# Performance work log

Hardware: AMD Instinct MI355X
Metric: run time of the kernel (lower is better)

Reference implementation:

```python
import jax, jax.numpy as jnp
import numpy as np

N_NODES = 50000
N_EDGES = 800000
HID = 128
EDGE_IN = 2 * HID + 4 + 20  # 2*hidden + edge_feat_dim + num_r_gaussian = 280


def setup_inputs() -> dict:
    key = jax.random.key(0)
    ks = jax.random.split(key, 16)
    s = lambda fan_in: 1.0 / np.sqrt(fan_in)
    inp = {
        "h": jax.random.normal(ks[0], (N_NODES, HID), dtype=jnp.float32),
        "edge_index": jax.random.randint(ks[1], (2, N_EDGES), 0, N_NODES, dtype=jnp.int64) if jax.config.jax_enable_x64 else jax.random.randint(ks[1], (2, N_EDGES), 0, N_NODES, dtype=jnp.int32),
        "edge_attr": jax.random.normal(ks[2], (N_EDGES, 24), dtype=jnp.float32),
        # edge_mlp: Linear(280->128) relu Linear(128->128) relu (act_last=True)
        "We1": jax.random.uniform(ks[3], (EDGE_IN, HID), jnp.float32, -s(EDGE_IN), s(EDGE_IN)),
        "be1": jnp.zeros((HID,), jnp.float32),
        "We2": jax.random.uniform(ks[4], (HID, HID), jnp.float32, -s(HID), s(HID)),
        "be2": jnp.zeros((HID,), jnp.float32),
        # edge_inf: Linear(128->1) + sigmoid
        "Wg": jax.random.uniform(ks[5], (HID, 1), jnp.float32, -s(HID), s(HID)),
        "bg": jnp.zeros((1,), jnp.float32),
        # node_mlp: Linear(256->128) relu Linear(128->128)
        "Wn1": jax.random.uniform(ks[6], (2 * HID, HID), jnp.float32, -s(2 * HID), s(2 * HID)),
        "bn1": jnp.zeros((HID,), jnp.float32),
        "Wn2": jax.random.uniform(ks[7], (HID, HID), jnp.float32, -s(HID), s(HID)),
        "bn2": jnp.zeros((HID,), jnp.float32),
    }
    return inp


def reference(h, edge_index, edge_attr, We1, be1, We2, be2, Wg, bg, Wn1, bn1, Wn2, bn2):
    dst, src = edge_index[0], edge_index[1]
    hi, hj = h[dst], h[src]                       # [E, HID] each
    x = jnp.concatenate([edge_attr, hi, hj], -1)  # [E, 280]
    mij = jax.nn.relu(jax.nn.relu(x @ We1 + be1) @ We2 + be2)  # [E, HID]
    eij = jax.nn.sigmoid(mij @ Wg + bg)           # [E, 1]
    mi = jax.ops.segment_sum(mij * eij, dst, num_segments=h.shape[0])  # [N, HID]
    y = jnp.concatenate([mi, h], -1)              # [N, 2*HID]
    out = jax.nn.relu(y @ Wn1 + bn1) @ Wn2 + bn2  # [N, HID]
    return out
```

## Files before the change

kernel.cpp:

```cpp
#include <hip/hip_runtime.h>

#define N_NODES 50000
#define N_EDGES 800000
#define HID 128

typedef _Float16 f16;
typedef _Float16 half8 __attribute__((ext_vector_type(8)));
typedef _Float16 half4 __attribute__((ext_vector_type(4)));
typedef _Float16 half2v __attribute__((ext_vector_type(2)));
typedef float f32x4 __attribute__((ext_vector_type(4)));
typedef float f32x2 __attribute__((ext_vector_type(2)));

#define OFF_MI     0UL
#define OFF_H16C   25600000UL
#define OFF_WC     38400000UL
#define OFF_CNT    38604800UL
#define OFF_CUR    38805504UL
#define OFF_E4     39006208UL
#define OFF_BT     51806208UL
#define CSR_TOTAL  51806464UL

#define OFF_FMI  0UL
#define OFF_FH16 25600000UL
#define OFF_FW   38400000UL

#define WB1 0
#define WB2 36864
#define WN1 53248
#define WN2 86016

#define TS 136
#define YS 264
#define AS 40

#define EB 64
#define NB 32

__global__ __launch_bounds__(256) void pack_weights(
    const float* __restrict__ We1, const float* __restrict__ We2,
    const float* __restrict__ Wn1, const float* __restrict__ Wn2,
    f16* __restrict__ W, int* __restrict__ cnt, float* __restrict__ mi) {
  int i = blockIdx.x * 256 + threadIdx.x;
  if (cnt && i < 50176) cnt[i] = 0;
  if (mi) {
    f32x4 z = {0.f, 0.f, 0.f, 0.f};
    for (int j = i; j < N_NODES * HID / 4; j += 102400)
      ((f32x4*)mi)[j] = z;
  }
  if (i < 36864) {
    int j = i & 7, n = (i >> 3) & 127, qk = i >> 10;
    int k = qk * 8 + j;
    float v = 0.f;
    if (k < 256) v = We1[(24 + k) * 128 + n];
    else if (k < 280) v = We1[(k - 256) * 128 + n];
    W[WB1 + i] = (f16)v;
  } else if (i < 53248) {
    int l = i - 36864;
    int j = l & 7, n = (l >> 3) & 127, qk = l >> 10;
    W[WB2 + l] = (f16)We2[(qk * 8 + j) * 128 + n];
  } else if (i < 86016) {
    int l = i - 53248;
    int j = l & 7, n = (l >> 3) & 127, qk = l >> 10;
    W[WN1 + l] = (f16)Wn1[(qk * 8 + j) * 128 + n];
  } else if (i < 102400) {
    int l = i - 86016;
    int j = l & 7, n = (l >> 3) & 127, qk = l >> 10;
    W[WN2 + l] = (f16)Wn2[(qk * 8 + j) * 128 + n];
  }
}

__global__ __launch_bounds__(256) void scanA(const int* __restrict__ cnt,
                                             int* __restrict__ cur, int* __restrict__ bt) {
  __shared__ int wsum[4];
  int t = threadIdx.x, b = blockIdx.x;
  int base = b * 1024 + t * 4;
  int4 v = *(const int4*)(cnt + base);
  int s = v.x + v.y + v.z + v.w;
  int lane = t & 63, w = t >> 6;
  int inc = s;
  #pragma unroll
  for (int off = 1; off < 64; off <<= 1) {
    int u = __shfl_up(inc, off, 64);
    if (lane >= off) inc += u;
  }
  if (lane == 63) wsum[w] = inc;
  __syncthreads();
  int wbase = 0;
  for (int i = 0; i < w; ++i) wbase += wsum[i];
  int excl = wbase + inc - s;
  int4 o;
  o.x = excl; o.y = excl + v.x; o.z = o.y + v.y; o.w = o.z + v.z;
  *(int4*)(cur + base) = o;
  if (t == 255) bt[b] = wbase + inc;
}

__global__ __launch_bounds__(256) void scanC(int* __restrict__ cur, const int* __restrict__ bt) {
  __shared__ int sbase;
  int t = threadIdx.x, b = blockIdx.x;
  if (t < 64) {
    int v = (t < b) ? bt[t] : 0;
    #pragma unroll
    for (int off = 32; off; off >>= 1) v += __shfl_down(v, off, 64);
    if (t == 0) sbase = v;
  }
  __syncthreads();
  int add = sbase;
  int base = b * 1024 + t * 4;
  int4 o = *(int4*)(cur + base);
  o.x += add; o.y += add; o.z += add; o.w += add;
  *(int4*)(cur + base) = o;
}

__global__ __launch_bounds__(256) void fill_perm(
    const int* __restrict__ eidx, int* __restrict__ cur, int4* __restrict__ e4) {
  int i = blockIdx.x * 256 + threadIdx.x;
  int d = eidx[i];
  int s = eidx[N_EDGES + i];
  int p = atomicAdd(&cur[d], 1);
  int4 rec; rec.x = i; rec.y = d; rec.z = s; rec.w = 0;
  e4[p] = rec;
}

__global__ __launch_bounds__(256, 8) void precompute_kernel(
    const float* __restrict__ h, const int* __restrict__ eidx,
    const f16* __restrict__ Wp, f16* __restrict__ P,
    f16* __restrict__ h16, int* __restrict__ cnt) {
  __shared__ f16 Y[NB * 136];
  int t = threadIdx.x;
  int n0 = blockIdx.x * NB;
  {
    int rb = t >> 4, ch = t & 15;
    #pragma unroll
    for (int p = 0; p < 2; ++p) {
      int r = p * 16 + rb;
      int g = n0 + r; if (g >= N_NODES) g = N_NODES - 1;
      const float4* s4 = (const float4*)(h + (size_t)g * HID + ch * 8);
      float4 a = s4[0], b = s4[1];
      half8 v = {(f16)a.x, (f16)a.y, (f16)a.z, (f16)a.w,
                 (f16)b.x, (f16)b.y, (f16)b.z, (f16)b.w};
      *(half8*)&Y[r * 136 + ch * 8] = v;
      *(half8*)(h16 + (size_t)g * HID + ch * 8) = v;
    }
  }
  if (cnt) {
    for (int i = blockIdx.x * 256 + t; i < N_EDGES; i += gridDim.x * 256)
      atomicAdd(&cnt[eidx[i]], 1);
  }
  __syncthreads();
  int w = t >> 6, lane = t & 63, q = lane >> 4, c = lane & 15;
  int colBase = w * 32;
  const f16* B = Wp + WB1 + ((size_t)(q * 128 + colBase + c)) * 8;
  f32x4 aD[2][2], aS[2][2];
  #pragma unroll
  for (int mt = 0; mt < 2; ++mt) {
    aD[mt][0] = (f32x4){0, 0, 0, 0}; aD[mt][1] = (f32x4){0, 0, 0, 0};
    aS[mt][0] = (f32x4){0, 0, 0, 0}; aS[mt][1] = (f32x4){0, 0, 0, 0};
  }
  #pragma unroll
  for (int ks = 0; ks < 4; ++ks) {
    half8 bD0 = *(const half8*)(B + ks * 4096);
    half8 bD1 = *(const half8*)(B + ks * 4096 + 128);
    half8 bS0 = *(const half8*)(B + (ks + 4) * 4096);
    half8 bS1 = *(const half8*)(B + (ks + 4) * 4096 + 128);
    #pragma unroll
    for (int mt = 0; mt < 2; ++mt) {
      half8 a = *(const half8*)&Y[(mt * 16 + c) * 136 + ks * 32 + q * 8];
      aD[mt][0] = __builtin_amdgcn_mfma_f32_16x16x32_f16(a, bD0, aD[mt][0], 0, 0, 0);
      aD[mt][1] = __builtin_amdgcn_mfma_f32_16x16x32_f16(a, bD1, aD[mt][1], 0, 0, 0);
      aS[mt][0] = __builtin_amdgcn_mfma_f32_16x16x32_f16(a, bS0, aS[mt][0], 0, 0, 0);
      aS[mt][1] = __builtin_amdgcn_mfma_f32_16x16x32_f16(a, bS1, aS[mt][1], 0, 0, 0);
    }
  }
  #pragma unroll
  for (int mt = 0; mt < 2; ++mt)
    #pragma unroll
    for (int r = 0; r < 4; ++r) {
      int g = n0 + mt * 16 + q * 4 + r;
      if (g < N_NODES) {
        f16* o = P + (size_t)g * 256 + colBase + c;
        o[0]        = (f16)aD[mt][0][r];
        o[16]       = (f16)aD[mt][1][r];
        o[128]      = (f16)aS[mt][0][r];
        o[128 + 16] = (f16)aS[mt][1][r];
      }
    }
}

__global__ __launch_bounds__(256, 6) void edge_kernel(
    const f16* __restrict__ P, const int* __restrict__ eidx,
    const float* __restrict__ eattr,
    const f16* __restrict__ Wp, const float* __restrict__ be1,
    const float* __restrict__ be2,
    const float* __restrict__ Wg, const float* __restrict__ bg,
    float* __restrict__ mi, const int4* __restrict__ e4) {
  __shared__ f16 S16[EB * TS];
  __shared__ f16 A[EB * AS];
  __shared__ float part[EB * 4];
  __shared__ float eijL[EB];
  __shared__ int dstL[EB];
  int t = threadIdx.x;
  int e0 = blockIdx.x * EB;

  if (t < EB) dstL[t] = e4 ? e4[e0 + t].y : eidx[e0 + t];

  {
    int rb = t >> 4, ch = t & 15;
    #pragma unroll
    for (int p = 0; p < 4; ++p) {
      int r = p * 16 + rb;
      int d, s;
      if (e4) {
        int4 rec = e4[e0 + r];
        d = rec.y; s = rec.z;
      } else {
        d = eidx[e0 + r]; s = eidx[N_EDGES + e0 + r];
      }
      half8 pd = *(const half8*)(P + (size_t)d * 256 + ch * 8);
      half8 ps = *(const half8*)(P + (size_t)s * 256 + 128 + ch * 8);
      *(half8*)&S16[r * TS + ch * 8] = pd + ps;
    }
  }
  for (int i = t; i < 384; i += 256) {
    int el = i / 6, kk = i % 6;
    int e = e4 ? e4[e0 + el].x : (e0 + el);
    float4 f = *(const float4*)(eattr + (size_t)e * 24 + kk * 4);
    half4 hv = {(f16)f.x, (f16)f.y, (f16)f.z, (f16)f.w};
    *(half4*)&A[el * AS + kk * 4] = hv;
  }
  if (t < EB) { uint4 z = {0, 0, 0, 0}; *(uint4*)&A[t * AS + 24] = z; }
  __syncthreads();

  int w = t >> 6, lane = t & 63, q = lane >> 4, c = lane & 15;
  int colBase = w * 32;

  f32x4 acc[4][2];
  {
    float b0 = be1[colBase + c], b1 = be1[colBase + 16 + c];
    #pragma unroll
    for (int mt = 0; mt < 4; ++mt) {
      acc[mt][0] = (f32x4){b0, b0, b0, b0};
      acc[mt][1] = (f32x4){b1, b1, b1, b1};
    }
  }
  {
    const f16* bA = Wp + WB1 + 32768 + ((size_t)(q * 128 + colBase + c)) * 8;
    half8 b0f = *(const half8*)(bA);
    half8 b1f = *(const half8*)(bA + 128);
    #pragma unroll
    for (int mt = 0; mt < 4; ++mt) {
      half8 a = *(const half8*)&A[(mt * 16 + c) * AS + q * 8];
      acc[mt][0] = __builtin_amdgcn_mfma_f32_16x16x32_f16(a, b0f, acc[mt][0], 0, 0, 0);
      acc[mt][1] = __builtin_amdgcn_mfma_f32_16x16x32_f16(a, b1f, acc[mt][1], 0, 0, 0);
    }
  }
  #pragma unroll
  for (int mt = 0; mt < 4; ++mt)
    #pragma unroll
    for (int r = 0; r < 4; ++r) {
      const f16* sr = &S16[(mt * 16 + q * 4 + r) * TS + colBase + c];
      acc[mt][0][r] += (float)sr[0];
      acc[mt][1][r] += (float)sr[16];
    }

  const f16* bp2base = Wp + WB2 + ((size_t)(q * 128 + colBase + c)) * 8;
  half8 d0 = *(const half8*)(bp2base);
  half8 d1 = *(const half8*)(bp2base + 128);

  __syncthreads();
  f16* T = S16;
  #pragma unroll
  for (int mt = 0; mt < 4; ++mt)
    #pragma unroll
    for (int nt = 0; nt < 2; ++nt)
      #pragma unroll
      for (int r = 0; r < 4; ++r) {
        float v = acc[mt][nt][r];
        T[(mt * 16 + q * 4 + r) * TS + colBase + nt * 16 + c] = (f16)(v > 0.f ? v : 0.f);
      }
  __syncthreads();

  f32x4 m2[4][2];
  {
    float b0 = be2[colBase + c], b1 = be2[colBase + 16 + c];
    #pragma unroll
    for (int mt = 0; mt < 4; ++mt) {
      m2[mt][0] = (f32x4){b0, b0, b0, b0};
      m2[mt][1] = (f32x4){b1, b1, b1, b1};
    }
  }
  #pragma unroll
  for (int kk = 0; kk < 4; ++kk) {
    half8 n0, n1;
    if (kk < 3) {
      n0 = *(const half8*)(bp2base + (kk + 1) * 4096);
      n1 = *(const half8*)(bp2base + (kk + 1) * 4096 + 128);
    }
    #pragma unroll
    for (int mt = 0; mt < 4; ++mt) {
      half8 a = *(const half8*)&T[(mt * 16 + c) * TS + kk * 32 + q * 8];
      m2[mt][0] = __builtin_amdgcn_mfma_f32_16x16x32_f16(a, d0, m2[mt][0], 0, 0, 0);
      m2[mt][1] = __builtin_amdgcn_mfma_f32_16x16x32_f16(a, d1, m2[mt][1], 0, 0, 0);
    }
    d0 = n0; d1 = n1;
  }

  float wg0 = Wg[colBase + c], wg1 = Wg[colBase + 16 + c];
  float pd[4][4];
  #pragma unroll
  for (int mt = 0; mt < 4; ++mt)
    #pragma unroll
    for (int r = 0; r < 4; ++r) {
      float v0 = m2[mt][0][r]; v0 = v0 > 0.f ? v0 : 0.f; m2[mt][0][r] = v0;
      float v1 = m2[mt][1][r]; v1 = v1 > 0.f ? v1 : 0.f; m2[mt][1][r] = v1;
      pd[mt][r] = v0 * wg0 + v1 * wg1;
    }
  #pragma unroll
  for (int off = 1; off < 16; off <<= 1)
    #pragma unroll
    for (int mt = 0; mt < 4; ++mt)
      #pragma unroll
      for (int r = 0; r < 4; ++r)
        pd[mt][r] += __shfl_xor(pd[mt][r], off, 64);
  if (c == 0)
    #pragma unroll
    for (int mt = 0; mt < 4; ++mt)
      #pragma unroll
      for (int r = 0; r < 4; ++r)
        part[(mt * 16 + q * 4 + r) * 4 + w] = pd[mt][r];
  __syncthreads();
  if (t < EB) {
    float s = part[t * 4] + part[t * 4 + 1] + part[t * 4 + 2] + part[t * 4 + 3] + bg[0];
    eijL[t] = 1.f / (1.f + __expf(-s));
  }
  __syncthreads();

  if (e4) {
    #pragma unroll
    for (int mt = 0; mt < 4; ++mt)
      #pragma unroll
      for (int r = 0; r < 4; ++r) {
        int el = mt * 16 + q * 4 + r;
        float ev = eijL[el];
        T[el * TS + colBase + c]      = (f16)(m2[mt][0][r] * ev);
        T[el * TS + colBase + 16 + c] = (f16)(m2[mt][1][r] * ev);
      }
    __syncthreads();
    int col = t & 127, half = t >> 7;
    int r0 = half * 32;
    float acc2 = 0.f;
    int dprev = dstL[r0];
    #pragma unroll
    for (int r2 = 0; r2 < 32; ++r2) {
      int rr = r0 + r2;
      acc2 += (float)T[rr * TS + col];
      int dnext = (r2 == 31) ? -1 : dstL[rr + 1];
      if (dnext != dprev) {
        atomicAdd(&mi[(size_t)dprev * HID + col], acc2);
        acc2 = 0.f;
        dprev = dnext;
      }
    }
  } else {
    #pragma unroll
    for (int mt = 0; mt < 4; ++mt)
      #pragma unroll
      for (int r = 0; r < 4; ++r) {
        int el = mt * 16 + q * 4 + r;
        float ev = eijL[el];
        float* base = mi + (size_t)dstL[el] * HID + colBase + c;
        atomicAdd(base,      m2[mt][0][r] * ev);
        atomicAdd(base + 16, m2[mt][1][r] * ev);
      }
  }
}

__global__ __launch_bounds__(256, 8) void node_kernel(
    const float* __restrict__ mi, const f16* __restrict__ h16,
    const f16* __restrict__ Wp, const float* __restrict__ bn1,
    const float* __restrict__ bn2, float* __restrict__ out) {
  __shared__ f16 Y[NB * YS];
  int t = threadIdx.x;
  int n0 = blockIdx.x * NB;
  {
    int rb = t >> 4, ch = t & 15;
    #pragma unroll
    for (int p = 0; p < 2; ++p) {
      int r = p * 16 + rb;
      int g = n0 + r; if (g >= N_NODES) g = N_NODES - 1;
      const float4* s = (const float4*)(mi + (size_t)g * HID + ch * 8);
      float4 a = s[0], b = s[1];
      half8 v = {(f16)a.x, (f16)a.y, (f16)a.z, (f16)a.w,
                 (f16)b.x, (f16)b.y, (f16)b.z, (f16)b.w};
      *(half8*)&Y[r * YS + ch * 8] = v;
      *(uint4*)&Y[r * YS + 128 + ch * 8] = *(const uint4*)(h16 + (size_t)g * HID + ch * 8);
    }
  }
  __syncthreads();
  int w = t >> 6, lane = t & 63, q = lane >> 4, c = lane & 15;
  int colBase = w * 32;
  const f16* BN1 = Wp + WN1;
  const f16* BN2 = Wp + WN2;
  f32x4 acc[2][2];
  {
    float b0 = bn1[colBase + c], b1 = bn1[colBase + 16 + c];
    #pragma unroll
    for (int mt = 0; mt < 2; ++mt) {
      acc[mt][0] = (f32x4){b0, b0, b0, b0};
      acc[mt][1] = (f32x4){b1, b1, b1, b1};
    }
  }
  const f16* bn1base = BN1 + ((size_t)(q * 128 + colBase + c)) * 8;
  half8 bf0 = *(const half8*)(bn1base);
  half8 bf1 = *(const half8*)(bn1base + 128);
  #pragma unroll
  for (int ks = 0; ks < 8; ++ks) {
    half8 nb0, nb1;
    if (ks < 7) {
      nb0 = *(const half8*)(bn1base + (ks + 1) * 4096);
      nb1 = *(const half8*)(bn1base + (ks + 1) * 4096 + 128);
    }
    #pragma unroll
    for (int mt = 0; mt < 2; ++mt) {
      half8 a = *(const half8*)&Y[(mt * 16 + c) * YS + ks * 32 + q * 8];
      acc[mt][0] = __builtin_amdgcn_mfma_f32_16x16x32_f16(a, bf0, acc[mt][0], 0, 0, 0);
      acc[mt][1] = __builtin_amdgcn_mfma_f32_16x16x32_f16(a, bf1, acc[mt][1], 0, 0, 0);
    }
    bf0 = nb0; bf1 = nb1;
  }
  const f16* bn2base = BN2 + ((size_t)(q * 128 + colBase + c)) * 8;
  half8 d0 = *(const half8*)(bn2base);
  half8 d1 = *(const half8*)(bn2base + 128);
  __syncthreads();
  f16* T = Y;
  #pragma unroll
  for (int mt = 0; mt < 2; ++mt)
    #pragma unroll
    for (int nt = 0; nt < 2; ++nt)
      #pragma unroll
      for (int r = 0; r < 4; ++r) {
        float v = acc[mt][nt][r];
        T[(mt * 16 + q * 4 + r) * TS + colBase + nt * 16 + c] = (f16)(v > 0.f ? v : 0.f);
      }
  __syncthreads();
  f32x4 m2[2][2];
  {
    float b0 = bn2[colBase + c], b1 = bn2[colBase + 16 + c];
    #pragma unroll
    for (int mt = 0; mt < 2; ++mt) {
      m2[mt][0] = (f32x4){b0, b0, b0, b0};
      m2[mt][1] = (f32x4){b1, b1, b1, b1};
    }
  }
  #pragma unroll
  for (int kk = 0; kk < 4; ++kk) {
    half8 n0, n1;
    if (kk < 3) {
      n0 = *(const half8*)(bn2base + (kk + 1) * 4096);
      n1 = *(const half8*)(bn2base + (kk + 1) * 4096 + 128);
    }
    #pragma unroll
    for (int mt = 0; mt < 2; ++mt) {
      half8 a = *(const half8*)&T[(mt * 16 + c) * TS + kk * 32 + q * 8];
      m2[mt][0] = __builtin_amdgcn_mfma_f32_16x16x32_f16(a, d0, m2[mt][0], 0, 0, 0);
      m2[mt][1] = __builtin_amdgcn_mfma_f32_16x16x32_f16(a, d1, m2[mt][1], 0, 0, 0);
    }
    d0 = n0; d1 = n1;
  }
  #pragma unroll
  for (int mt = 0; mt < 2; ++mt)
    #pragma unroll
    for (int r = 0; r < 4; ++r) {
      int g = n0 + mt * 16 + q * 4 + r;
      if (g < N_NODES) {
        float* o = out + (size_t)g * HID + colBase + c;
        o[0]  = m2[mt][0][r];
        o[16] = m2[mt][1][r];
      }
    }
}

extern "C" void kernel_launch(void* const* d_in, const int* in_sizes, int n_in,
                              void* d_out, int out_size, void* d_ws, size_t ws_size,
                              hipStream_t stream) {
  const float* h    = (const float*)d_in[0];
  const int*   eidx = (const int*)d_in[1];
  const float* eattr= (const float*)d_in[2];
  const float* We1  = (const float*)d_in[3];
  const float* be1  = (const float*)d_in[4];
  const float* We2  = (const float*)d_in[5];
  const float* be2  = (const float*)d_in[6];
  const float* Wg   = (const float*)d_in[7];
  const float* bg   = (const float*)d_in[8];
  const float* Wn1  = (const float*)d_in[9];
  const float* bn1  = (const float*)d_in[10];
  const float* Wn2  = (const float*)d_in[11];
  const float* bn2  = (const float*)d_in[12];
  float* out = (float*)d_out;
  char* ws = (char*)d_ws;

  if (ws_size >= CSR_TOTAL) {
    float* mi  = (float*)(ws + OFF_MI);
    f16* h16   = (f16*)(ws + OFF_H16C);
    f16* Wp    = (f16*)(ws + OFF_WC);
    int* cnt   = (int*)(ws + OFF_CNT);
    int* cur   = (int*)(ws + OFF_CUR);
    int4* e4   = (int4*)(ws + OFF_E4);
    int* bt    = (int*)(ws + OFF_BT);
    f16* P     = (f16*)out;

    pack_weights<<<400, 256, 0, stream>>>(We1, We2, Wn1, Wn2, Wp, cnt, mi);
    precompute_kernel<<<(N_NODES + NB - 1) / NB, 256, 0, stream>>>(h, eidx, Wp, P, h16, cnt);
    scanA<<<49, 256, 0, stream>>>(cnt, cur, bt);
    scanC<<<49, 256, 0, stream>>>(cur, bt);
    fill_perm<<<3125, 256, 0, stream>>>(eidx, cur, e4);
    edge_kernel<<<N_EDGES / EB, 256, 0, stream>>>(P, eidx, eattr, Wp, be1, be2,
                                                  Wg, bg, mi, e4);
    node_kernel<<<(N_NODES + NB - 1) / NB, 256, 0, stream>>>(mi, h16, Wp, bn1, bn2, out);
  } else {
    float* mi  = (float*)(ws + OFF_FMI);
    f16*   h16 = (f16*)(ws + OFF_FH16);
    f16*   Wp  = (f16*)(ws + OFF_FW);
    f16*   P   = (f16*)out;

    pack_weights<<<400, 256, 0, stream>>>(We1, We2, Wn1, Wn2, Wp, nullptr, mi);
    precompute_kernel<<<(N_NODES + NB - 1) / NB, 256, 0, stream>>>(h, eidx, Wp, P, h16, nullptr);
    edge_kernel<<<N_EDGES / EB, 256, 0, stream>>>(P, eidx, eattr, Wp, be1, be2,
                                                  Wg, bg, mi, nullptr);
    node_kernel<<<(N_NODES + NB - 1) / NB, 256, 0, stream>>>(mi, h16, Wp, bn1, bn2, out);
  }
}
```

Before: 400.3 us.

## Halve edge tile, swizzle block order, merge scan kernels into one pass

Edge tiles shrink from 64 to 32 edges per block, and launch bounds rise to allow 8 waves-groups per CU. The block index is remapped so consecutive blocks take strided regions of the sorted edge list. The two-kernel prefix scan becomes a single kernel in which each block recomputes the sum of the preceding counts itself, removing one launch. The segmented atomic reduction now uses half2 reads over 8-row groups. Smaller tiles can mean more atomics per destination and less weight reuse per block.

```diff
diff --git a/kernel.cpp b/kernel.cpp
--- a/kernel.cpp
+++ b/kernel.cpp
@@ -17,8 +17,7 @@
 #define OFF_CNT    38604800UL
 #define OFF_CUR    38805504UL
 #define OFF_E4     39006208UL
-#define OFF_BT     51806208UL
-#define CSR_TOTAL  51806464UL
+#define CSR_TOTAL  51806208UL
 
 #define OFF_FMI  0UL
 #define OFF_FH16 25600000UL
@@ -33,7 +32,7 @@
 #define YS 264
 #define AS 40
 
-#define EB 64
+#define EB 32
 #define NB 32
 
 __global__ __launch_bounds__(256) void pack_weights(
@@ -69,14 +68,25 @@
   }
 }
 
-__global__ __launch_bounds__(256) void scanA(const int* __restrict__ cnt,
-                                             int* __restrict__ cur, int* __restrict__ bt) {
+__global__ __launch_bounds__(256) void scan_kernel(const int* __restrict__ cnt,
+                                                   int* __restrict__ cur) {
+  __shared__ int red[4];
   __shared__ int wsum[4];
   int t = threadIdx.x, b = blockIdx.x;
+  int lane = t & 63, w = t >> 6;
+  int s0 = 0;
+  for (int i = t * 4; i < b * 1024; i += 1024) {
+    int4 v = *(const int4*)(cnt + i);
+    s0 += v.x + v.y + v.z + v.w;
+  }
+  #pragma unroll
+  for (int off = 32; off; off >>= 1) s0 += __shfl_down(s0, off, 64);
+  if (lane == 0) red[w] = s0;
+  __syncthreads();
+  int base_all = red[0] + red[1] + red[2] + red[3];
   int base = b * 1024 + t * 4;
   int4 v = *(const int4*)(cnt + base);
   int s = v.x + v.y + v.z + v.w;
-  int lane = t & 63, w = t >> 6;
   int inc = s;
   #pragma unroll
   for (int off = 1; off < 64; off <<= 1) {
@@ -87,27 +97,9 @@
   __syncthreads();
   int wbase = 0;
   for (int i = 0; i < w; ++i) wbase += wsum[i];
-  int excl = wbase + inc - s;
+  int excl = base_all + wbase + inc - s;
   int4 o;
   o.x = excl; o.y = excl + v.x; o.z = o.y + v.y; o.w = o.z + v.z;
-  *(int4*)(cur + base) = o;
-  if (t == 255) bt[b] = wbase + inc;
-}
-
-__global__ __launch_bounds__(256) void scanC(int* __restrict__ cur, const int* __restrict__ bt) {
-  __shared__ int sbase;
-  int t = threadIdx.x, b = blockIdx.x;
-  if (t < 64) {
-    int v = (t < b) ? bt[t] : 0;
-    #pragma unroll
-    for (int off = 32; off; off >>= 1) v += __shfl_down(v, off, 64);
-    if (t == 0) sbase = v;
-  }
-  __syncthreads();
-  int add = sbase;
-  int base = b * 1024 + t * 4;
-  int4 o = *(int4*)(cur + base);
-  o.x += add; o.y += add; o.z += add; o.w += add;
   *(int4*)(cur + base) = o;
 }
 
@@ -186,7 +178,7 @@
     }
 }
 
-__global__ __launch_bounds__(256, 6) void edge_kernel(
+__global__ __launch_bounds__(256, 8) void edge_kernel(
     const f16* __restrict__ P, const int* __restrict__ eidx,
     const float* __restrict__ eattr,
     const f16* __restrict__ Wp, const float* __restrict__ be1,
@@ -199,14 +191,15 @@
   __shared__ float eijL[EB];
   __shared__ int dstL[EB];
   int t = threadIdx.x;
-  int e0 = blockIdx.x * EB;
+  int bid = (blockIdx.x & 7) * 3125 + (blockIdx.x >> 3);
+  int e0 = bid * EB;
 
   if (t < EB) dstL[t] = e4 ? e4[e0 + t].y : eidx[e0 + t];
 
   {
     int rb = t >> 4, ch = t & 15;
     #pragma unroll
-    for (int p = 0; p < 4; ++p) {
+    for (int p = 0; p < 2; ++p) {
       int r = p * 16 + rb;
       int d, s;
       if (e4) {
@@ -220,8 +213,8 @@
       *(half8*)&S16[r * TS + ch * 8] = pd + ps;
     }
   }
-  for (int i = t; i < 384; i += 256) {
-    int el = i / 6, kk = i % 6;
+  if (t < 192) {
+    int el = t / 6, kk = t % 6;
     int e = e4 ? e4[e0 + el].x : (e0 + el);
     float4 f = *(const float4*)(eattr + (size_t)e * 24 + kk * 4);
     half4 hv = {(f16)f.x, (f16)f.y, (f16)f.z, (f16)f.w};
@@ -233,11 +226,11 @@
   int w = t >> 6, lane = t & 63, q = lane >> 4, c = lane & 15;
   int colBase = w * 32;
 
-  f32x4 acc[4][2];
+  f32x4 acc[2][2];
   {
     float b0 = be1[colBase + c], b1 = be1[colBase + 16 + c];
     #pragma unroll
-    for (int mt = 0; mt < 4; ++mt) {
+    for (int mt = 0; mt < 2; ++mt) {
       acc[mt][0] = (f32x4){b0, b0, b0, b0};
       acc[mt][1] = (f32x4){b1, b1, b1, b1};
     }
@@ -247,14 +240,14 @@
     half8 b0f = *(const half8*)(bA);
     half8 b1f = *(const half8*)(bA + 128);
     #pragma unroll
-    for (int mt = 0; mt < 4; ++mt) {
+    for (int mt = 0; mt < 2; ++mt) {
       half8 a = *(const half8*)&A[(mt * 16 + c) * AS + q * 8];
       acc[mt][0] = __builtin_amdgcn_mfma_f32_16x16x32_f16(a, b0f, acc[mt][0], 0, 0, 0);
       acc[mt][1] = __builtin_amdgcn_mfma_f32_16x16x32_f16(a, b1f, acc[mt][1], 0, 0, 0);
     }
   }
   #pragma unroll
-  for (int mt = 0; mt < 4; ++mt)
+  for (int mt = 0; mt < 2; ++mt)
     #pragma unroll
     for (int r = 0; r < 4; ++r) {
       const f16* sr = &S16[(mt * 16 + q * 4 + r) * TS + colBase + c];
@@ -269,7 +262,7 @@
   __syncthreads();
   f16* T = S16;
   #pragma unroll
-  for (int mt = 0; mt < 4; ++mt)
+  for (int mt = 0; mt < 2; ++mt)
     #pragma unroll
     for (int nt = 0; nt < 2; ++nt)
       #pragma unroll
@@ -279,11 +272,11 @@
       }
   __syncthreads();
 
-  f32x4 m2[4][2];
+  f32x4 m2[2][2];
   {
     float b0 = be2[colBase + c], b1 = be2[colBase + 16 + c];
     #pragma unroll
-    for (int mt = 0; mt < 4; ++mt) {
+    for (int mt = 0; mt < 2; ++mt) {
       m2[mt][0] = (f32x4){b0, b0, b0, b0};
       m2[mt][1] = (f32x4){b1, b1, b1, b1};
     }
@@ -296,7 +289,7 @@
       n1 = *(const half8*)(bp2base + (kk + 1) * 4096 + 128);
     }
     #pragma unroll
-    for (int mt = 0; mt < 4; ++mt) {
+    for (int mt = 0; mt < 2; ++mt) {
       half8 a = *(const half8*)&T[(mt * 16 + c) * TS + kk * 32 + q * 8];
       m2[mt][0] = __builtin_amdgcn_mfma_f32_16x16x32_f16(a, d0, m2[mt][0], 0, 0, 0);
       m2[mt][1] = __builtin_amdgcn_mfma_f32_16x16x32_f16(a, d1, m2[mt][1], 0, 0, 0);
@@ -305,9 +298,9 @@
   }
 
   float wg0 = Wg[colBase + c], wg1 = Wg[colBase + 16 + c];
-  float pd[4][4];
-  #pragma unroll
-  for (int mt = 0; mt < 4; ++mt)
+  float pd[2][4];
+  #pragma unroll
+  for (int mt = 0; mt < 2; ++mt)
     #pragma unroll
     for (int r = 0; r < 4; ++r) {
       float v0 = m2[mt][0][r]; v0 = v0 > 0.f ? v0 : 0.f; m2[mt][0][r] = v0;
@@ -317,13 +310,13 @@
   #pragma unroll
   for (int off = 1; off < 16; off <<= 1)
     #pragma unroll
-    for (int mt = 0; mt < 4; ++mt)
+    for (int mt = 0; mt < 2; ++mt)
       #pragma unroll
       for (int r = 0; r < 4; ++r)
         pd[mt][r] += __shfl_xor(pd[mt][r], off, 64);
   if (c == 0)
     #pragma unroll
-    for (int mt = 0; mt < 4; ++mt)
+    for (int mt = 0; mt < 2; ++mt)
       #pragma unroll
       for (int r = 0; r < 4; ++r)
         part[(mt * 16 + q * 4 + r) * 4 + w] = pd[mt][r];
@@ -336,7 +329,7 @@
 
   if (e4) {
     #pragma unroll
-    for (int mt = 0; mt < 4; ++mt)
+    for (int mt = 0; mt < 2; ++mt)
       #pragma unroll
       for (int r = 0; r < 4; ++r) {
         int el = mt * 16 + q * 4 + r;
@@ -345,24 +338,25 @@
         T[el * TS + colBase + 16 + c] = (f16)(m2[mt][1][r] * ev);
       }
     __syncthreads();
-    int col = t & 127, half = t >> 7;
-    int r0 = half * 32;
-    float acc2 = 0.f;
+    int cp = t & 63, grp = t >> 6;
+    int r0 = grp * 8;
+    float ax = 0.f, ay = 0.f;
     int dprev = dstL[r0];
     #pragma unroll
-    for (int r2 = 0; r2 < 32; ++r2) {
+    for (int r2 = 0; r2 < 8; ++r2) {
       int rr = r0 + r2;
-      acc2 += (float)T[rr * TS + col];
-      int dnext = (r2 == 31) ? -1 : dstL[rr + 1];
+      half2v v = *(const half2v*)&T[rr * TS + 2 * cp];
+      ax += (float)v[0]; ay += (float)v[1];
+      int dnext = (r2 == 7) ? -1 : dstL[rr + 1];
       if (dnext != dprev) {
-        atomicAdd(&mi[(size_t)dprev * HID + col], acc2);
-        acc2 = 0.f;
-        dprev = dnext;
+        float* base = &mi[(size_t)dprev * HID + 2 * cp];
+        atomicAdd(base, ax); atomicAdd(base + 1, ay);
+        ax = 0.f; ay = 0.f; dprev = dnext;
       }
     }
   } else {
     #pragma unroll
-    for (int mt = 0; mt < 4; ++mt)
+    for (int mt = 0; mt < 2; ++mt)
       #pragma unroll
       for (int r = 0; r < 4; ++r) {
         int el = mt * 16 + q * 4 + r;
@@ -505,13 +499,11 @@
     int* cnt   = (int*)(ws + OFF_CNT);
     int* cur   = (int*)(ws + OFF_CUR);
     int4* e4   = (int4*)(ws + OFF_E4);
-    int* bt    = (int*)(ws + OFF_BT);
     f16* P     = (f16*)out;
 
     pack_weights<<<400, 256, 0, stream>>>(We1, We2, Wn1, Wn2, Wp, cnt, mi);
     precompute_kernel<<<(N_NODES + NB - 1) / NB, 256, 0, stream>>>(h, eidx, Wp, P, h16, cnt);
-    scanA<<<49, 256, 0, stream>>>(cnt, cur, bt);
-    scanC<<<49, 256, 0, stream>>>(cur, bt);
+    scan_kernel<<<49, 256, 0, stream>>>(cnt, cur);
     fill_perm<<<3125, 256, 0, stream>>>(eidx, cur, e4);
     edge_kernel<<<N_EDGES / EB, 256, 0, stream>>>(P, eidx, eattr, Wp, be1, be2,
                                                   Wg, bg, mi, e4);
```

New measurement: 425.5 us. +6.3%, slower.
